# Kernel tuning notes

Hardware: AMD Instinct MI355X
Metric: run time of the kernel (lower is better)

Reference implementation:

```python
import jax, jax.numpy as jnp
import numpy as np

NUM_HEADS = 16
EPS = 1e-5
CHUNK = 128  # chunk length for the chunked recurrent-state scan


def _linear_attention(x, Wq, Wk, Wv, Wo, bo):
    B, T, E = x.shape
    H = NUM_HEADS
    d = E // H

    def proj(W):
        # nn.Linear(bias=False): y = x @ W.T ; split heads -> (B,H,T,d)
        return (x @ W.T).reshape(B, T, H, d).transpose(0, 2, 1, 3)

    phi_q = jax.nn.elu(proj(Wq)) + 1.0
    phi_k = jax.nn.elu(proj(Wk)) + 1.0
    V = proj(Wv)

    nC = T // CHUNK
    # (nC, B, H, C, d) so lax.scan iterates over chunks of time
    def to_chunks(a):
        return a.reshape(B, H, nC, CHUNK, d).transpose(2, 0, 1, 3, 4)

    qc, kc, vc = to_chunks(phi_q), to_chunks(phi_k), to_chunks(V)
    mask = jnp.tril(jnp.ones((CHUNK, CHUNK), x.dtype))  # causal incl. diagonal

    S0 = jnp.zeros((B, H, d, d), x.dtype)  # running sum of k v^T
    z0 = jnp.zeros((B, H, d), x.dtype)     # running sum of phi_k

    def step(carry, inp):
        S, z = carry
        q, k, v = inp  # (B,H,C,d)
        A = jnp.einsum('bhid,bhjd->bhij', q, k) * mask
        num = jnp.einsum('bhij,bhjd->bhid', A, v) + jnp.einsum('bhid,bhde->bhie', q, S)
        den = jnp.sum(A, axis=-1) + jnp.einsum('bhid,bhd->bhi', q, z) + EPS
        out = num / den[..., None]
        S = S + jnp.einsum('bhjd,bhje->bhde', k, v)
        z = z + jnp.sum(k, axis=2)
        return (S, z), out

    _, outs = jax.lax.scan(step, (S0, z0), (qc, kc, vc))  # (nC,B,H,C,d)
    out = outs.transpose(1, 2, 0, 3, 4).reshape(B, H, T, d)
    out = out.transpose(0, 2, 1, 3).reshape(B, T, E)
    # out_proj (dropout p=0 / eval -> identity)
    return out @ Wo.T + bo


def setup_inputs() -> dict:
    key = jax.random.key(0)
    ks = jax.random.split(key, 6)
    B, T, E = 2, 2048, 1024
    s = 1.0 / np.sqrt(E)
    return {
        'x': jax.random.normal(ks[0], (B, T, E), jnp.float32),
        'Wq': jax.random.normal(ks[1], (E, E), jnp.float32) * s,
        'Wk': jax.random.normal(ks[2], (E, E), jnp.float32) * s,
        'Wv': jax.random.normal(ks[3], (E, E), jnp.float32) * s,
        'Wo': jax.random.normal(ks[4], (E, E), jnp.float32) * s,
        'bo': jnp.zeros((E,), jnp.float32),
    }


def reference(x, Wq, Wk, Wv, Wo, bo):
    return _linear_attention(x, Wq, Wk, Wv, Wo, bo)
```

## Files before the change

kernel.cpp:

```cpp
#include <hip/hip_runtime.h>
#include <hip/hip_bf16.h>
#include <stdint.h>

typedef __attribute__((ext_vector_type(4)))  float  floatx4;
typedef __attribute__((ext_vector_type(8)))  short  short8;
typedef __attribute__((ext_vector_type(8)))  unsigned short ushortx8;
typedef __attribute__((ext_vector_type(4)))  unsigned short ushortx4;

#define B_  2
#define T_  2048
#define E_  1024
#define H_  16
#define D_  64
#define C_  128
#define NC_ 16
#define M_  4096
#define EPS_ 1e-5f

__device__ __forceinline__ unsigned short f2b(float f) {
    union { float f; unsigned int u; } v; v.f = f;
    unsigned int r = v.u + 0x7fffu + ((v.u >> 16) & 1u);
    return (unsigned short)(r >> 16);
}
__device__ __forceinline__ float b2f(unsigned short b) {
    union { unsigned int u; float f; } v; v.u = ((unsigned int)b) << 16;
    return v.f;
}

__device__ __forceinline__ int stage_seg(int i) { return (i & 3) ^ ((i >> 3) & 3); }
__device__ __forceinline__ int frag_slot(int lane) {
    int m = lane & 15, q = lane >> 4;
    return m * 4 + (q ^ ((m >> 1) & 3));
}

__global__ __launch_bounds__(256) void convert_all(const float* __restrict__ x,
                                                   const float* __restrict__ Wq,
                                                   const float* __restrict__ Wk,
                                                   const float* __restrict__ Wv,
                                                   const float* __restrict__ Wo,
                                                   unsigned short* __restrict__ dst) {
    int i = (blockIdx.x * 256 + threadIdx.x) * 4;
    const float* s; int off;
    if (i < M_ * E_) { s = x; off = i; }
    else {
        int j = i - M_ * E_;
        int which = j >> 20;
        s = (which == 0) ? Wq : (which == 1) ? Wk : (which == 2) ? Wv : Wo;
        off = j & ((1 << 20) - 1);
    }
    float4 f = *(const float4*)(s + off);
    ushortx4 o;
    o[0] = f2b(f.x); o[1] = f2b(f.y); o[2] = f2b(f.z); o[3] = f2b(f.w);
    *(ushortx4*)(dst + i) = o;
}

__global__ __launch_bounds__(256) void gemm_qkv(const unsigned short* __restrict__ A,
                                                const unsigned short* __restrict__ Bm,
                                                unsigned short* __restrict__ Cb) {
    const int N = 3 * E_, K = E_;
    __shared__ __align__(16) unsigned short smem[16384];
    unsigned short* at = smem;
    unsigned short* bt = smem + 8192;
    int tid = threadIdx.x;
    int wave = tid >> 6, lane = tid & 63;
    int wr = wave >> 1, wc = wave & 1;
    int m = lane & 15, q = lane >> 4;
    int srow = lane >> 2, sseg = stage_seg(lane);
    int fs = frag_slot(lane);
    int row0 = blockIdx.y * 128, col0 = blockIdx.x * 128;
    floatx4 acc[4][4];
    for (int i = 0; i < 4; i++) for (int j = 0; j < 4; j++) acc[i][j] = floatx4{0.f, 0.f, 0.f, 0.f};

    for (int k0 = 0; k0 < K; k0 += 64) {
        __syncthreads();
        for (int p = 0; p < 4; p++) {
            int t = p * 4 + wave;
            const unsigned short* ga = A + (size_t)(row0 + (t & 7) * 16 + srow) * K + k0 + (t >> 3) * 32 + sseg * 8;
            __builtin_amdgcn_global_load_lds((const __attribute__((address_space(1))) unsigned int*)ga,
                (__attribute__((address_space(3))) unsigned int*)(at + t * 512), 16, 0, 0);
        }
        for (int p = 0; p < 4; p++) {
            int u = p * 4 + wave;
            const unsigned short* gb = Bm + (size_t)(col0 + (u & 7) * 16 + srow) * K + k0 + (u >> 3) * 32 + sseg * 8;
            __builtin_amdgcn_global_load_lds((const __attribute__((address_space(1))) unsigned int*)gb,
                (__attribute__((address_space(3))) unsigned int*)(bt + u * 512), 16, 0, 0);
        }
        __syncthreads();
        for (int kh = 0; kh < 2; kh++) {
            short8 af[4], bf[4];
            for (int mi = 0; mi < 4; mi++) af[mi] = *(const short8*)(at + (kh * 8 + wr * 4 + mi) * 512 + fs * 8);
            for (int ni = 0; ni < 4; ni++) bf[ni] = *(const short8*)(bt + (kh * 8 + wc * 4 + ni) * 512 + fs * 8);
            for (int mi = 0; mi < 4; mi++)
                for (int ni = 0; ni < 4; ni++)
                    acc[mi][ni] = __builtin_amdgcn_mfma_f32_16x16x32_bf16(af[mi], bf[ni], acc[mi][ni], 0, 0, 0);
        }
    }

    __syncthreads();
    unsigned short* epi = smem + wave * 2176;
    bool isphi = (col0 < 2 * E_);
    for (int half = 0; half < 2; half++) {
        if (half) asm volatile("" ::: "memory");
        for (int mi2 = 0; mi2 < 2; mi2++) {
            int mi = half * 2 + mi2;
            for (int ni = 0; ni < 4; ni++)
                for (int reg = 0; reg < 4; reg++) {
                    int lr = mi2 * 16 + q * 4 + reg;
                    float v = acc[mi][ni][reg];
                    if (isphi) v = (v > 0.f) ? (v + 1.f) : __expf(v);
                    epi[lr * 68 + ni * 16 + m] = f2b(v);
                }
        }
        for (int i = 0; i < 4; i++) {
            int s = i * 64 + lane;
            int lr = s >> 3, seg = s & 7;
            const unsigned short* p = epi + lr * 68 + seg * 8;
            ushortx4 lo = *(const ushortx4*)(p);
            ushortx4 hi = *(const ushortx4*)(p + 4);
            ushortx8 val;
            for (int e = 0; e < 4; e++) { val[e] = lo[e]; val[e + 4] = hi[e]; }
            int row = row0 + wr * 64 + half * 32 + lr;
            int col = col0 + wc * 64 + seg * 8;
            *(ushortx8*)(Cb + (size_t)row * N + col) = val;
        }
    }
}

__global__ __launch_bounds__(256) void gemm_out(const unsigned short* __restrict__ A,
                                                const unsigned short* __restrict__ Bm,
                                                const float* __restrict__ bias,
                                                float* __restrict__ Cf) {
    const int N = E_, K = E_;
    __shared__ __align__(16) unsigned short at[16 * 512];
    __shared__ __align__(16) unsigned short bt[8 * 512];
    int tid = threadIdx.x;
    int wave = tid >> 6, lane = tid & 63;
    int wr = wave >> 1, wc = wave & 1;
    int m = lane & 15, q = lane >> 4;
    int srow = lane >> 2, sseg = stage_seg(lane);
    int fs = frag_slot(lane);
    int row0 = blockIdx.y * 128, col0 = blockIdx.x * 64;
    floatx4 acc[4][2];
    for (int i = 0; i < 4; i++) for (int j = 0; j < 2; j++) acc[i][j] = floatx4{0.f, 0.f, 0.f, 0.f};

    for (int k0 = 0; k0 < K; k0 += 64) {
        __syncthreads();
        for (int p = 0; p < 4; p++) {
            int t = p * 4 + wave;
            const unsigned short* ga = A + (size_t)(row0 + (t & 7) * 16 + srow) * K + k0 + (t >> 3) * 32 + sseg * 8;
            __builtin_amdgcn_global_load_lds((const __attribute__((address_space(1))) unsigned int*)ga,
                (__attribute__((address_space(3))) unsigned int*)(at + t * 512), 16, 0, 0);
        }
        for (int p = 0; p < 2; p++) {
            int u = p * 4 + wave;
            const unsigned short* gb = Bm + (size_t)(col0 + (u & 3) * 16 + srow) * K + k0 + (u >> 2) * 32 + sseg * 8;
            __builtin_amdgcn_global_load_lds((const __attribute__((address_space(1))) unsigned int*)gb,
                (__attribute__((address_space(3))) unsigned int*)(bt + u * 512), 16, 0, 0);
        }
        __syncthreads();
        for (int kh = 0; kh < 2; kh++) {
            short8 af[4], bf[2];
            for (int mi = 0; mi < 4; mi++) af[mi] = *(const short8*)(at + (kh * 8 + wr * 4 + mi) * 512 + fs * 8);
            for (int ci = 0; ci < 2; ci++) bf[ci] = *(const short8*)(bt + (kh * 4 + wc * 2 + ci) * 512 + fs * 8);
            for (int mi = 0; mi < 4; mi++)
                for (int ci = 0; ci < 2; ci++)
                    acc[mi][ci] = __builtin_amdgcn_mfma_f32_16x16x32_bf16(af[mi], bf[ci], acc[mi][ci], 0, 0, 0);
        }
    }
    int qrow = q * 4;
    for (int ci = 0; ci < 2; ci++) {
        int col = col0 + wc * 32 + ci * 16 + m;
        float bv = bias[col];
        for (int mi = 0; mi < 4; mi++)
            for (int r2 = 0; r2 < 4; r2++) {
                int row = row0 + wr * 64 + mi * 16 + qrow + r2;
                Cf[(size_t)row * N + col] = acc[mi][ci][r2] + bv;
            }
    }
}

__global__ __launch_bounds__(256) void chunk_sums(const unsigned short* __restrict__ qkv,
                                                  float* __restrict__ Sc, float* __restrict__ zc) {
    int c = blockIdx.x, h = blockIdx.y, bb = blockIdx.z;
    __shared__ __align__(16) unsigned short Kt[64 * 132];
    __shared__ __align__(16) unsigned short Vt[80 * 132];
    int tid = threadIdx.x;
    int lane = tid & 63, w = tid >> 6;
    size_t rowb = (size_t)bb * T_ + (size_t)c * C_;
    int kcol = E_ + h * D_, vcol = 2 * E_ + h * D_;

    {
        int r4 = (tid >> 3) * 4;
        int seg = (tid & 7) * 8;
        ushortx8 kv[4], vv[4];
        for (int t = 0; t < 4; t++) {
            size_t g = (rowb + r4 + t) * 3072;
            kv[t] = *(const ushortx8*)(qkv + g + kcol + seg);
            vv[t] = *(const ushortx8*)(qkv + g + vcol + seg);
        }
        for (int e = 0; e < 8; e++) {
            ushortx4 ka, va;
            for (int t = 0; t < 4; t++) { ka[t] = kv[t][e]; va[t] = vv[t][e]; }
            *(ushortx4*)(Kt + (seg + e) * 132 + r4) = ka;
            *(ushortx4*)(Vt + (seg + e) * 132 + r4) = va;
        }
    }
    if (tid < 128) Vt[64 * 132 + tid] = 0x3f80;
    __syncthreads();

    floatx4 acc[5];
    for (int ni = 0; ni < 5; ni++) acc[ni] = floatx4{0.f, 0.f, 0.f, 0.f};
    int lm = lane & 15, lk = (lane >> 4) * 8;
    for (int k0 = 0; k0 < 128; k0 += 32) {
        short8 af = *(const short8*)(Kt + (w * 16 + lm) * 132 + k0 + lk);
        for (int ni = 0; ni < 5; ni++) {
            short8 bf = *(const short8*)(Vt + (ni * 16 + lm) * 132 + k0 + lk);
            acc[ni] = __builtin_amdgcn_mfma_f32_16x16x32_bf16(af, bf, acc[ni], 0, 0, 0);
        }
    }
    size_t base = ((size_t)(bb * H_ + h) * NC_ + c) * (size_t)(D_ * D_);
    int r0 = w * 16 + (lane >> 4) * 4;
    for (int ni = 0; ni < 4; ni++)
        for (int reg = 0; reg < 4; reg++)
            Sc[base + (size_t)(r0 + reg) * D_ + ni * 16 + lm] = acc[ni][reg];
    if (lm == 0) {
        size_t zb = ((size_t)(bb * H_ + h) * NC_ + c) * D_;
        for (int reg = 0; reg < 4; reg++) zc[zb + r0 + reg] = acc[4][reg];
    }
}

__global__ __launch_bounds__(256) void attn_kernel(const unsigned short* __restrict__ qkv,
                                                   const float* __restrict__ Sc,
                                                   const float* __restrict__ zc,
                                                   unsigned short* __restrict__ attn) {
    int c = blockIdx.x, h = blockIdx.y, bb = blockIdx.z;
    __shared__ __align__(16) unsigned short qs[128 * 68];
    __shared__ __align__(16) unsigned short ks[128 * 68];
    __shared__ __align__(16) unsigned short vt[64 * 132];
    __shared__ __align__(16) unsigned short ovl[128 * 36];
    __shared__ float zsh[64];
    int tid = threadIdx.x;
    int lane = tid & 63, w = tid >> 6;
    int lm = lane & 15, lq = lane >> 4;
    size_t rowb = (size_t)bb * T_ + (size_t)c * C_;
    int qcol = h * D_, kcol = E_ + h * D_, vcol = 2 * E_ + h * D_;

    for (int s = 0; s < 4; s++) {
        int off = s * 256 + tid;
        int r = off >> 3, seg = (off & 7) * 8;
        size_t g = (rowb + r) * 3072;
        ushortx8 q8 = *(const ushortx8*)(qkv + g + qcol + seg);
        ushortx8 k8 = *(const ushortx8*)(qkv + g + kcol + seg);
        *(ushortx8*)(qs + r * 68 + seg) = q8;
        *(ushortx8*)(ks + r * 68 + seg) = k8;
    }
    {
        int r4 = (tid >> 3) * 4;
        int seg = (tid & 7) * 8;
        ushortx8 vv[4];
        for (int t = 0; t < 4; t++)
            vv[t] = *(const ushortx8*)(qkv + (rowb + r4 + t) * 3072 + vcol + seg);
        for (int e = 0; e < 8; e++) {
            ushortx4 va;
            for (int t = 0; t < 4; t++) va[t] = vv[t][e];
            *(ushortx4*)(vt + (seg + e) * 132 + r4) = va;
        }
    }
    {
        size_t scb = ((size_t)(bb * H_ + h) * NC_) * (size_t)(D_ * D_);
        int p = tid * 16;
        float a[16];
        for (int i = 0; i < 16; i++) a[i] = 0.f;
        for (int j = 0; j < c; j++) {
            const float* Sj = Sc + scb + (size_t)j * (D_ * D_) + p;
            for (int q = 0; q < 16; q += 4) {
                float4 f = *(const float4*)(Sj + q);
                a[q] += f.x; a[q + 1] += f.y; a[q + 2] += f.z; a[q + 3] += f.w;
            }
        }
        for (int i = 0; i < 16; i++) {
            int d = (p + i) >> 6, e = (p + i) & 63;
            ovl[e * 68 + d] = f2b(a[i]);
        }
    }
    if (tid < 64) {
        size_t zb = ((size_t)(bb * H_ + h) * NC_) * D_;
        float zr = 0.f;
        for (int j = 0; j < c; j++) zr += zc[zb + (size_t)j * D_ + tid];
        zsh[tid] = zr;
    }
    __syncthreads();

    floatx4 acc[2][4];
    for (int mi = 0; mi < 2; mi++) for (int ni = 0; ni < 4; ni++) acc[mi][ni] = floatx4{0.f, 0.f, 0.f, 0.f};
    for (int k0 = 0; k0 < 64; k0 += 32) {
        short8 aq[2];
        for (int mi = 0; mi < 2; mi++)
            aq[mi] = *(const short8*)(qs + (w * 32 + mi * 16 + lm) * 68 + k0 + lq * 8);
        for (int ni = 0; ni < 4; ni++) {
            short8 bs = *(const short8*)(ovl + (ni * 16 + lm) * 68 + k0 + lq * 8);
            for (int mi = 0; mi < 2; mi++)
                acc[mi][ni] = __builtin_amdgcn_mfma_f32_16x16x32_bf16(aq[mi], bs, acc[mi][ni], 0, 0, 0);
        }
    }
    float dsum[2][4];
    {
        int d0 = lm * 4;
        float4 z4 = *(const float4*)(zsh + d0);
        for (int mi = 0; mi < 2; mi++)
            for (int reg = 0; reg < 4; reg++) {
                int row = w * 32 + mi * 16 + lq * 4 + reg;
                ushortx4 q4 = *(const ushortx4*)(qs + row * 68 + d0);
                dsum[mi][reg] = b2f(q4[0]) * z4.x + b2f(q4[1]) * z4.y + b2f(q4[2]) * z4.z + b2f(q4[3]) * z4.w;
            }
    }
    __syncthreads();

    for (int jt = 0; jt <= w; jt++) {
        floatx4 pa[2][2];
        for (int mi = 0; mi < 2; mi++) for (int ct = 0; ct < 2; ct++) pa[mi][ct] = floatx4{0.f, 0.f, 0.f, 0.f};
        for (int k0 = 0; k0 < 64; k0 += 32) {
            short8 aq[2];
            for (int mi = 0; mi < 2; mi++)
                aq[mi] = *(const short8*)(qs + (w * 32 + mi * 16 + lm) * 68 + k0 + lq * 8);
            for (int ct = 0; ct < 2; ct++) {
                short8 bk = *(const short8*)(ks + (jt * 32 + ct * 16 + lm) * 68 + k0 + lq * 8);
                for (int mi = 0; mi < 2; mi++)
                    pa[mi][ct] = __builtin_amdgcn_mfma_f32_16x16x32_bf16(aq[mi], bk, pa[mi][ct], 0, 0, 0);
            }
        }
        bool diag = (jt == w);
        for (int mi = 0; mi < 2; mi++)
            for (int ct = 0; ct < 2; ct++)
                for (int reg = 0; reg < 4; reg++) {
                    int il = mi * 16 + lq * 4 + reg;
                    int jl = ct * 16 + lm;
                    float v = pa[mi][ct][reg];
                    if (diag && jl > il) v = 0.f;
                    dsum[mi][reg] += v;
                    ovl[(w * 32 + il) * 36 + jl] = f2b(v);
                }
        short8 ap[2];
        for (int mi = 0; mi < 2; mi++)
            ap[mi] = *(const short8*)(ovl + (w * 32 + mi * 16 + lm) * 36 + lq * 8);
        for (int ni = 0; ni < 4; ni++) {
            short8 bv = *(const short8*)(vt + (ni * 16 + lm) * 132 + jt * 32 + lq * 8);
            for (int mi = 0; mi < 2; mi++)
                acc[mi][ni] = __builtin_amdgcn_mfma_f32_16x16x32_bf16(ap[mi], bv, acc[mi][ni], 0, 0, 0);
        }
    }

    for (int off = 1; off < 16; off <<= 1)
        for (int mi = 0; mi < 2; mi++)
            for (int reg = 0; reg < 4; reg++)
                dsum[mi][reg] += __shfl_xor(dsum[mi][reg], off);

    for (int mi = 0; mi < 2; mi++)
        for (int reg = 0; reg < 4; reg++) {
            float inv = 1.f / (dsum[mi][reg] + EPS_);
            int row = w * 32 + mi * 16 + lq * 4 + reg;
            for (int ni = 0; ni < 4; ni++)
                attn[(rowb + row) * E_ + h * D_ + ni * 16 + lm] = f2b(acc[mi][ni][reg] * inv);
        }
}

extern "C" void kernel_launch(void* const* d_in, const int* in_sizes, int n_in,
                              void* d_out, int out_size, void* d_ws, size_t ws_size,
                              hipStream_t stream) {
    const float* x  = (const float*)d_in[0];
    const float* Wq = (const float*)d_in[1];
    const float* Wk = (const float*)d_in[2];
    const float* Wv = (const float*)d_in[3];
    const float* Wo = (const float*)d_in[4];
    const float* bo = (const float*)d_in[5];
    float* out = (float*)d_out;

    const size_t MB = 1024 * 1024;
    uint8_t* ws = (uint8_t*)d_ws;
    unsigned short* xb    = (unsigned short*)(ws + 0);
    unsigned short* wb    = (unsigned short*)(ws + 8 * MB);
    unsigned short* wob   = wb + 3 * E_ * E_;
    unsigned short* qkvb  = (unsigned short*)(ws + 16 * MB);
    float* Sc = (float*)(ws + 40 * MB);
    float* zc = (float*)(ws + 48 * MB);
    unsigned short* attnb = xb;

    convert_all<<<(M_ * E_ + 4 * E_ * E_) / 1024, 256, 0, stream>>>(x, Wq, Wk, Wv, Wo, xb);

    gemm_qkv<<<dim3(24, 32), 256, 0, stream>>>(xb, wb, qkvb);
    chunk_sums<<<dim3(NC_, H_, B_), 256, 0, stream>>>(qkvb, Sc, zc);
    attn_kernel<<<dim3(NC_, H_, B_), 256, 0, stream>>>(qkvb, Sc, zc, attnb);
    gemm_out<<<dim3(16, 32), 256, 0, stream>>>(attnb, wob, bo, out);
}
```

Baseline: 171.7 us.

## Double-buffer LDS staging in QKV and output projection GEMMs

Both projection GEMMs now use two LDS buffers, so the async global-to-LDS load of the next K tile is issued before the MFMA compute on the current tile. This halves the number of barriers per K step and is meant to hide global memory latency behind compute. In exchange, LDS use per block doubles (64 KB for the QKV GEMM), which may reduce occupancy.

Result: faster. 167.4 us (-2.5%).

```diff
diff --git a/kernel.cpp b/kernel.cpp
--- a/kernel.cpp
+++ b/kernel.cpp
@@ -58,9 +58,11 @@
                                                 const unsigned short* __restrict__ Bm,
                                                 unsigned short* __restrict__ Cb) {
     const int N = 3 * E_, K = E_;
-    __shared__ __align__(16) unsigned short smem[16384];
-    unsigned short* at = smem;
-    unsigned short* bt = smem + 8192;
+    __shared__ __align__(16) unsigned short smem[32768];
+    unsigned short* at0 = smem;
+    unsigned short* bt0 = smem + 8192;
+    unsigned short* at1 = smem + 16384;
+    unsigned short* bt1 = smem + 24576;
     int tid = threadIdx.x;
     int wave = tid >> 6, lane = tid & 63;
     int wr = wave >> 1, wc = wave & 1;
@@ -71,8 +73,7 @@
     floatx4 acc[4][4];
     for (int i = 0; i < 4; i++) for (int j = 0; j < 4; j++) acc[i][j] = floatx4{0.f, 0.f, 0.f, 0.f};
 
-    for (int k0 = 0; k0 < K; k0 += 64) {
-        __syncthreads();
+    auto stage = [&](unsigned short* at, unsigned short* bt, int k0) {
         for (int p = 0; p < 4; p++) {
             int t = p * 4 + wave;
             const unsigned short* ga = A + (size_t)(row0 + (t & 7) * 16 + srow) * K + k0 + (t >> 3) * 32 + sseg * 8;
@@ -85,7 +86,8 @@
             __builtin_amdgcn_global_load_lds((const __attribute__((address_space(1))) unsigned int*)gb,
                 (__attribute__((address_space(3))) unsigned int*)(bt + u * 512), 16, 0, 0);
         }
-        __syncthreads();
+    };
+    auto compute = [&](const unsigned short* at, const unsigned short* bt) {
         for (int kh = 0; kh < 2; kh++) {
             short8 af[4], bf[4];
             for (int mi = 0; mi < 4; mi++) af[mi] = *(const short8*)(at + (kh * 8 + wr * 4 + mi) * 512 + fs * 8);
@@ -94,9 +96,19 @@
                 for (int ni = 0; ni < 4; ni++)
                     acc[mi][ni] = __builtin_amdgcn_mfma_f32_16x16x32_bf16(af[mi], bf[ni], acc[mi][ni], 0, 0, 0);
         }
-    }
-
+    };
+
+    stage(at0, bt0, 0);
     __syncthreads();
+    for (int k0 = 0; k0 < K; k0 += 128) {
+        stage(at1, bt1, k0 + 64);
+        compute(at0, bt0);
+        __syncthreads();
+        if (k0 + 128 < K) stage(at0, bt0, k0 + 128);
+        compute(at1, bt1);
+        __syncthreads();
+    }
+
     unsigned short* epi = smem + wave * 2176;
     bool isphi = (col0 < 2 * E_);
     for (int half = 0; half < 2; half++) {
@@ -131,8 +143,11 @@
                                                 const float* __restrict__ bias,
                                                 float* __restrict__ Cf) {
     const int N = E_, K = E_;
-    __shared__ __align__(16) unsigned short at[16 * 512];
-    __shared__ __align__(16) unsigned short bt[8 * 512];
+    __shared__ __align__(16) unsigned short smem[24576];
+    unsigned short* at0 = smem;
+    unsigned short* bt0 = smem + 8192;
+    unsigned short* at1 = smem + 12288;
+    unsigned short* bt1 = smem + 20480;
     int tid = threadIdx.x;
     int wave = tid >> 6, lane = tid & 63;
     int wr = wave >> 1, wc = wave & 1;
@@ -143,8 +158,7 @@
     floatx4 acc[4][2];
     for (int i = 0; i < 4; i++) for (int j = 0; j < 2; j++) acc[i][j] = floatx4{0.f, 0.f, 0.f, 0.f};
 
-    for (int k0 = 0; k0 < K; k0 += 64) {
-        __syncthreads();
+    auto stage = [&](unsigned short* at, unsigned short* bt, int k0) {
         for (int p = 0; p < 4; p++) {
             int t = p * 4 + wave;
             const unsigned short* ga = A + (size_t)(row0 + (t & 7) * 16 + srow) * K + k0 + (t >> 3) * 32 + sseg * 8;
@@ -157,7 +171,8 @@
             __builtin_amdgcn_global_load_lds((const __attribute__((address_space(1))) unsigned int*)gb,
                 (__attribute__((address_space(3))) unsigned int*)(bt + u * 512), 16, 0, 0);
         }
-        __syncthreads();
+    };
+    auto compute = [&](const unsigned short* at, const unsigned short* bt) {
         for (int kh = 0; kh < 2; kh++) {
             short8 af[4], bf[2];
             for (int mi = 0; mi < 4; mi++) af[mi] = *(const short8*)(at + (kh * 8 + wr * 4 + mi) * 512 + fs * 8);
@@ -166,7 +181,19 @@
                 for (int ci = 0; ci < 2; ci++)
                     acc[mi][ci] = __builtin_amdgcn_mfma_f32_16x16x32_bf16(af[mi], bf[ci], acc[mi][ci], 0, 0, 0);
         }
-    }
+    };
+
+    stage(at0, bt0, 0);
+    __syncthreads();
+    for (int k0 = 0; k0 < K; k0 += 128) {
+        stage(at1, bt1, k0 + 64);
+        compute(at0, bt0);
+        __syncthreads();
+        if (k0 + 128 < K) stage(at0, bt0, k0 + 128);
+        compute(at1, bt1);
+        __syncthreads();
+    }
+
     int qrow = q * 4;
     for (int ci = 0; ci < 2; ci++) {
         int col = col0 + wc * 32 + ci * 16 + m;
```
